# Performance work log

Measured on AMD Instinct MI355X. Metric: run time of the kernel, lower is better.

Reference implementation:

```python
import jax, jax.numpy as jnp
import numpy as np

N_USER = 100000
N_ITEM = 50000
N_EDGE = 400000
D_IN = 128
N_HEADS = 4
D_HEAD = 32


def setup_inputs() -> dict:
    key = jax.random.key(0)
    ks = jax.random.split(key, 10)
    s = 1.0 / np.sqrt(D_IN)
    return {
        "h_user": jax.random.normal(ks[0], (N_USER, D_IN), jnp.float32),
        "h_item": jax.random.normal(ks[1], (N_ITEM, D_IN), jnp.float32),
        "edge_user": jax.random.randint(ks[2], (N_EDGE,), 0, N_USER),
        "edge_item": jax.random.randint(ks[3], (N_EDGE,), 0, N_ITEM),
        "user_w_qs": jax.random.normal(ks[4], (N_HEADS, D_IN, D_HEAD), jnp.float32) * s,
        "user_w_ks": jax.random.normal(ks[5], (N_HEADS, D_IN, D_HEAD), jnp.float32) * s,
        "user_w_vs": jax.random.normal(ks[6], (N_HEADS, D_IN, D_HEAD), jnp.float32) * s,
        "item_w_qs": jax.random.normal(ks[7], (N_HEADS, D_IN, D_HEAD), jnp.float32) * s,
        "item_w_ks": jax.random.normal(ks[8], (N_HEADS, D_IN, D_HEAD), jnp.float32) * s,
        "item_w_vs": jax.random.normal(ks[9], (N_HEADS, D_IN, D_HEAD), jnp.float32) * s,
    }


def _segment_softmax(logit, seg, num_segments):
    m = jax.ops.segment_max(logit, seg, num_segments=num_segments)
    e = jnp.exp(logit - m[seg])
    s = jax.ops.segment_sum(e, seg, num_segments=num_segments)
    return e / s[seg]


def _attend(src_idx, dst_idx, h_src, h_dst, w_qs, w_ks, w_vs, n_dst):
    # per-head projections: [H, n, d_head]
    q = jnp.einsum("nd,hde->hne", h_dst, w_qs)
    k = jnp.einsum("nd,hde->hne", h_src, w_ks)
    v = jnp.einsum("nd,hde->hne", h_src, w_vs)
    # per-edge logits: [H, E]
    logit = jnp.sum(q[:, dst_idx] * k[:, src_idx], axis=-1)
    att = jax.vmap(lambda l: _segment_softmax(l, dst_idx, n_dst))(logit)
    # sparse adj @ v == segment-sum of attention-weighted source values
    msg = att[..., None] * v[:, src_idx]  # [H, E, d_head]
    z = jax.vmap(lambda m: jax.ops.segment_sum(m, dst_idx, num_segments=n_dst))(msg)
    z = jax.nn.relu(z)  # nonlinear per head, then merge (concat)
    return jnp.transpose(z, (1, 0, 2)).reshape(n_dst, -1)


def reference(h_user, h_item, edge_user, edge_item,
              user_w_qs, user_w_ks, user_w_vs,
              item_w_qs, item_w_ks, item_w_vs):
    # i2u: items -> users (dst = users)
    z_user = _attend(edge_item, edge_user, h_item, h_user,
                     user_w_qs, item_w_ks, item_w_vs, N_USER)
    # u2i: users -> items (dst = items)
    z_item = _attend(edge_user, edge_item, h_user, h_item,
                     item_w_qs, user_w_ks, user_w_vs, N_ITEM)
    return (z_user, z_item)
```

## Files before the change

### kernel.cpp

```cpp
#include <hip/hip_runtime.h>
#include <hip/hip_fp16.h>


typedef unsigned short u16;
typedef float f32x4 __attribute__((ext_vector_type(4)));
typedef short bf16x8 __attribute__((ext_vector_type(8)));

#define NU_C    100000
#define NI_C    50000
#define E_C     400000
#define D_IN    128
#define D_HEAD  32
#define N_HEADS 4

#define PROJ_ROWS 64

#define SCAN_T  256
#define SCAN_E  1024

__device__ __forceinline__ float bf2f(u16 b) {
    return __uint_as_float(((unsigned)b) << 16);
}

__device__ __forceinline__ u16 f2bf_rn(float x) {
    unsigned u = __float_as_uint(x);
    u += 0x7FFFu + ((u >> 16) & 1u);
    return (u16)(u >> 16);
}

__device__ __forceinline__ u16 f2h(float x) {
    return __half_as_ushort(__float2half(x));
}
__device__ __forceinline__ float h2f(u16 b) {
    return __half2float(__ushort_as_half(b));
}

__global__ void detect_dtypes(const void* __restrict__ h,
                              const void* __restrict__ eu,
                              int* __restrict__ flags) {
    if (threadIdx.x != 0 || blockIdx.x != 0) return;
    const u16* hw = (const u16*)h;
    int cnt = 0;
    for (int i = 0; i < 128; ++i) {
        unsigned ex = (hw[2 * i] >> 7) & 0xFFu;
        if (ex >= 118u && ex <= 137u) cnt++;
    }
    flags[0] = (cnt >= 64) ? 1 : 0;
    const int* ew = (const int*)eu;
    int nz = 0;
    for (int i = 0; i < 256; ++i)
        if (ew[2 * i + 1] != 0) nz++;
    flags[1] = (nz == 0) ? 1 : 0;
    flags[2] = 0;
    flags[3] = 0;
}

__global__ void decode_hist(const int* __restrict__ e_user,
                            const int* __restrict__ e_item,
                            int* __restrict__ du, int* __restrict__ di,
                            int* __restrict__ degU, int* __restrict__ degI,
                            int* __restrict__ flags) {
    int g = blockIdx.x * 256 + threadIdx.x;
    if (g >= E_C) return;
    int is64 = flags[1];
    int u = is64 ? e_user[2 * g] : e_user[g];
    int i = is64 ? e_item[2 * g] : e_item[g];
    if ((unsigned)u >= (unsigned)NU_C) { atomicOr(&flags[3], 1); u = 0; }
    if ((unsigned)i >= (unsigned)NI_C) { atomicOr(&flags[3], 1); i = 0; }
    du[g] = u;
    di[g] = i;
    atomicAdd(&degU[u], 1);
    atomicAdd(&degI[i], 1);
}

__global__ __launch_bounds__(256)
void wtrans(const void* __restrict__ w0, const void* __restrict__ w1,
            const void* __restrict__ w2, const void* __restrict__ w3,
            const void* __restrict__ w4, const void* __restrict__ w5,
            u16* __restrict__ wthi, u16* __restrict__ wtlo,
            const int* __restrict__ flags) {
    int b = blockIdx.x;
    int m = b >> 6;
    int f = (b & 63) * 256 + threadIdx.x;
    const void* ws[6] = { w0, w1, w2, w3, w4, w5 };
    const void* wp = ws[m];
    int head = f >> 12, d = (f >> 5) & 127, e = f & 31;
    float x;
    if (flags[0]) x = bf2f(((const u16*)wp)[f]);
    else          x = ((const float*)wp)[f];
    u16 h = f2bf_rn(x);
    u16 l = f2bf_rn(x - bf2f(h));
    int o = m * 16384 + (head * 32 + e) * 128 + d;
    wthi[o] = h;
    wtlo[o] = l;
}

__global__ __launch_bounds__(SCAN_T)
void scan_pass1(const int* __restrict__ degU, int* __restrict__ offsU,
                int* __restrict__ partU, int nU, int sbU,
                const int* __restrict__ degI, int* __restrict__ offsI,
                int* __restrict__ partI, int nI) {
    __shared__ int tsum[SCAN_T];
    int t = threadIdx.x, b = blockIdx.x;
    const int* deg; int* offs; int* partials; int n; int lb;
    if (b < sbU) { deg = degU; offs = offsU; partials = partU; n = nU; lb = b; }
    else         { deg = degI; offs = offsI; partials = partI; n = nI; lb = b - sbU; }
    int idx = lb * SCAN_E + t * 4;
    int v0 = 0, v1 = 0, v2 = 0, v3 = 0;
    if (idx + 3 < n) {
        v0 = deg[idx]; v1 = deg[idx + 1]; v2 = deg[idx + 2]; v3 = deg[idx + 3];
    } else {
        if (idx     < n) v0 = deg[idx];
        if (idx + 1 < n) v1 = deg[idx + 1];
        if (idx + 2 < n) v2 = deg[idx + 2];
        if (idx + 3 < n) v3 = deg[idx + 3];
    }
    int s = v0 + v1 + v2 + v3;
    tsum[t] = s;
    __syncthreads();
#pragma unroll
    for (int o = 1; o < SCAN_T; o <<= 1) {
        int x = (t >= o) ? tsum[t - o] : 0;
        __syncthreads();
        tsum[t] += x;
        __syncthreads();
    }
    int run = tsum[t] - s;
    if (idx     < n) offs[idx]     = run;             run += v0;
    if (idx + 1 < n) offs[idx + 1] = run;             run += v1;
    if (idx + 2 < n) offs[idx + 2] = run;             run += v2;
    if (idx + 3 < n) offs[idx + 3] = run;
    if (t == SCAN_T - 1) partials[lb] = tsum[t];
}

__global__ __launch_bounds__(SCAN_T)
void scan_pass2(int* __restrict__ partU, int sbU, int* __restrict__ offsU, int nU,
                int* __restrict__ partI, int sbI, int* __restrict__ offsI, int nI) {
    __shared__ int tsum[SCAN_T];
    int t = threadIdx.x;
    int* partials; int nb; int* offs; int n;
    if (blockIdx.x == 0) { partials = partU; nb = sbU; offs = offsU; n = nU; }
    else                 { partials = partI; nb = sbI; offs = offsI; n = nI; }
    int v = (t < nb) ? partials[t] : 0;
    tsum[t] = v;
    __syncthreads();
#pragma unroll
    for (int o = 1; o < SCAN_T; o <<= 1) {
        int x = (t >= o) ? tsum[t - o] : 0;
        __syncthreads();
        tsum[t] += x;
        __syncthreads();
    }
    if (t < nb) partials[t] = tsum[t] - v;
    if (t == SCAN_T - 1) offs[n] = tsum[t];
}

__global__ __launch_bounds__(SCAN_T)
void scan_pass3(int* __restrict__ offsU, const int* __restrict__ partU,
                int nU, int sbU,
                int* __restrict__ offsI, const int* __restrict__ partI, int nI) {
    int t = threadIdx.x, b = blockIdx.x;
    int* offs; const int* partials; int n; int lb;
    if (b < sbU) { offs = offsU; partials = partU; n = nU; lb = b; }
    else         { offs = offsI; partials = partI; n = nI; lb = b - sbU; }
    int add = partials[lb];
    int idx = lb * SCAN_E + t * 4;
#pragma unroll
    for (int i = 0; i < 4; ++i)
        if (idx + i < n) offs[idx + i] += add;
}

__global__ void scatter2(const int* __restrict__ du, const int* __restrict__ di,
                         const int* __restrict__ offsU, int* __restrict__ cntU,
                         int* __restrict__ csrU,
                         const int* __restrict__ offsI, int* __restrict__ cntI,
                         int* __restrict__ csrI, int egrid) {
    int b = blockIdx.x;
    int g = (b >= egrid ? b - egrid : b) * 256 + threadIdx.x;
    if (g >= E_C) return;
    if (b < egrid) {
        int d = du[g];
        int pos = offsU[d] + atomicAdd(&cntU[d], 1);
        csrU[pos] = di[g];
    } else {
        int d = di[g];
        int pos = offsI[d] + atomicAdd(&cntI[d], 1);
        csrI[pos] = du[g];
    }
}

__global__ __launch_bounds__(256)
void proj3(const void* __restrict__ h0, const u16* __restrict__ wth0,
           const u16* __restrict__ wtl0, u16* __restrict__ o0, int N0, int pg0,
           const void* __restrict__ h1, const u16* __restrict__ wth1,
           const u16* __restrict__ wtl1, u16* __restrict__ o1, int N1, int pg1,
           const void* __restrict__ h2, const u16* __restrict__ wth2,
           const u16* __restrict__ wtl2, u16* __restrict__ o2, int N2,
           const int* __restrict__ flags) {
    __shared__ u16 Hhi[PROJ_ROWS * 32], Hlo[PROJ_ROWS * 32];
    __shared__ u16 Bhi[128 * 32],       Blo[128 * 32];

    const int b = blockIdx.x;
    const void* hraw; const u16* wth; const u16* wtl; u16* out; int N; int lb;
    if (b < pg0)            { hraw = h0; wth = wth0; wtl = wtl0; out = o0; N = N0; lb = b; }
    else if (b < pg0 + pg1) { hraw = h1; wth = wth1; wtl = wtl1; out = o1; N = N1; lb = b - pg0; }
    else                    { hraw = h2; wth = wth2; wtl = wtl2; out = o2; N = N2; lb = b - pg0 - pg1; }

    const int t = threadIdx.x;
    const int n0 = lb * PROJ_ROWS;
    const int isbf = flags[0];

    const int srow = t >> 2, sq = t & 3;
    const int sgn = min(n0 + srow, N - 1);
    const int hbase = srow * 32 + ((sq ^ ((srow >> 1) & 3)) << 3);
    const int wj = t >> 1, wh = t & 1;
    const int wb0 = wj * 32 + (((wh * 2)     ^ ((wj >> 1) & 3)) << 3);
    const int wb1 = wj * 32 + (((wh * 2 + 1) ^ ((wj >> 1) & 3)) << 3);
    const int w = t >> 6, l = t & 63;
    const int lr = l & 15, lk = l >> 4;
    const int sc = (lk ^ ((lr >> 1) & 3)) << 3;

    f32x4 acc[4][2];
#pragma unroll
    for (int rt = 0; rt < 4; ++rt)
#pragma unroll
        for (int ci = 0; ci < 2; ++ci) {
            acc[rt][ci].x = 0.f; acc[rt][ci].y = 0.f;
            acc[rt][ci].z = 0.f; acc[rt][ci].w = 0.f;
        }

#define COMPUTE_STEP                                                           \
    do {                                                                       \
        bf16x8 fAh[4], fAl[4], fBh[2], fBl[2];                                 \
        _Pragma("unroll")                                                      \
        for (int rt = 0; rt < 4; ++rt) {                                       \
            int ar = (rt * 16 + lr) * 32 + sc;                                 \
            fAh[rt] = *(const bf16x8*)&Hhi[ar];                                \
            fAl[rt] = *(const bf16x8*)&Hlo[ar];                                \
        }                                                                      \
        _Pragma("unroll")                                                      \
        for (int ci = 0; ci < 2; ++ci) {                                       \
            int jr = ((w * 2 + ci) * 16 + lr) * 32 + sc;                       \
            fBh[ci] = *(const bf16x8*)&Bhi[jr];                                \
            fBl[ci] = *(const bf16x8*)&Blo[jr];                                \
        }                                                                      \
        _Pragma("unroll")                                                      \
        for (int rt = 0; rt < 4; ++rt)                                         \
        _Pragma("unroll")                                                      \
        for (int ci = 0; ci < 2; ++ci) {                                       \
            acc[rt][ci] = __builtin_amdgcn_mfma_f32_16x16x32_bf16(             \
                fAl[rt], fBh[ci], acc[rt][ci], 0, 0, 0);                       \
            acc[rt][ci] = __builtin_amdgcn_mfma_f32_16x16x32_bf16(             \
                fAh[rt], fBl[ci], acc[rt][ci], 0, 0, 0);                       \
            acc[rt][ci] = __builtin_amdgcn_mfma_f32_16x16x32_bf16(             \
                fAh[rt], fBh[ci], acc[rt][ci], 0, 0, 0);                       \
        }                                                                      \
    } while (0)

    if (!isbf) {
        const float* hp = (const float*)hraw;
        f32x4 rh0, rh1; bf16x8 rwh0, rwh1, rwl0, rwl1;
#define PLOAD(KC)                                                              \
        do {                                                                   \
            const float* hq = hp + (size_t)sgn * D_IN + (KC) * 32 + sq * 8;    \
            rh0 = *(const f32x4*)hq;                                           \
            rh1 = *(const f32x4*)(hq + 4);                                     \
            const u16* wp = wth + wj * 128 + (KC) * 32 + wh * 16;              \
            rwh0 = *(const bf16x8*)wp;  rwh1 = *(const bf16x8*)(wp + 8);       \
            const u16* lp = wtl + wj * 128 + (KC) * 32 + wh * 16;              \
            rwl0 = *(const bf16x8*)lp;  rwl1 = *(const bf16x8*)(lp + 8);       \
        } while (0)
        PLOAD(0);
        for (int kc = 0; kc < 4; ++kc) {
            if (kc) __syncthreads();
            bf16x8 hi8, lo8;
#pragma unroll
            for (int i = 0; i < 4; ++i) {
                u16 hh = f2bf_rn(rh0[i]);
                hi8[i] = (short)hh;
                lo8[i] = (short)f2bf_rn(rh0[i] - bf2f(hh));
            }
#pragma unroll
            for (int i = 0; i < 4; ++i) {
                u16 hh = f2bf_rn(rh1[i]);
                hi8[4 + i] = (short)hh;
                lo8[4 + i] = (short)f2bf_rn(rh1[i] - bf2f(hh));
            }
            *(bf16x8*)&Hhi[hbase] = hi8;
            *(bf16x8*)&Hlo[hbase] = lo8;
            *(bf16x8*)&Bhi[wb0] = rwh0;
            *(bf16x8*)&Bhi[wb1] = rwh1;
            *(bf16x8*)&Blo[wb0] = rwl0;
            *(bf16x8*)&Blo[wb1] = rwl1;
            __syncthreads();
            if (kc < 3) PLOAD(kc + 1);
            COMPUTE_STEP;
        }
#undef PLOAD
    } else {
        for (int kc = 0; kc < 4; ++kc) {
            if (kc) __syncthreads();
            bf16x8 hv = *(const bf16x8*)((const u16*)hraw
                        + (size_t)sgn * D_IN + kc * 32 + sq * 8);
            bf16x8 z;
#pragma unroll
            for (int i = 0; i < 8; ++i) z[i] = 0;
            *(bf16x8*)&Hhi[hbase] = hv;
            *(bf16x8*)&Hlo[hbase] = z;
            const u16* wp = wth + wj * 128 + kc * 32 + wh * 16;
            const u16* lp = wtl + wj * 128 + kc * 32 + wh * 16;
            *(bf16x8*)&Bhi[wb0] = *(const bf16x8*)wp;
            *(bf16x8*)&Bhi[wb1] = *(const bf16x8*)(wp + 8);
            *(bf16x8*)&Blo[wb0] = *(const bf16x8*)lp;
            *(bf16x8*)&Blo[wb1] = *(const bf16x8*)(lp + 8);
            __syncthreads();
            COMPUTE_STEP;
        }
    }
#undef COMPUTE_STEP

#pragma unroll
    for (int rt = 0; rt < 4; ++rt) {
#pragma unroll
        for (int r = 0; r < 4; ++r) {
            int n = n0 + rt * 16 + lk * 4 + r;
            if (n < N) {
#pragma unroll
                for (int ci = 0; ci < 2; ++ci)
                    out[(size_t)n * 128 + w * 32 + ci * 16 + lr] =
                        f2h(acc[rt][ci][r]);
            }
        }
    }
}

__global__ __launch_bounds__(256)
void gather64(const int* __restrict__ offs, const int* __restrict__ csr,
              const u16* __restrict__ q,
              const u16* __restrict__ k,
              const u16* __restrict__ v,
              float* __restrict__ out,
              int Ndst, const int* __restrict__ flags) {
    int g = blockIdx.x * 256 + threadIdx.x;
    int dst = g >> 6;
    if (dst >= Ndst) return;
    int l  = g & 63;
    int eh = l >> 5;
    int sl = l & 31;
    float* op = out + (size_t)dst * 128 + sl * 4;

    if (flags[3]) {
        if (eh == 0) {
            f32x4 d64; d64.x = d64.y = d64.z = d64.w = 64.0f;
            *(f32x4*)op = d64;
        }
        return;
    }

    ushort4 qu = *(const ushort4*)(q + (size_t)dst * 128 + sl * 4);
    f32x4 qv;
    qv.x = h2f(qu.x); qv.y = h2f(qu.y); qv.z = h2f(qu.z); qv.w = h2f(qu.w);
    f32x4 acc; acc.x = acc.y = acc.z = acc.w = 0.f;
    float ssum = 0.f;

    int e0 = offs[dst], e1 = offs[dst + 1];
    int e = e0 + eh;
    for (; e + 2 < e1; e += 4) {
        int s0 = csr[e];
        int s1 = csr[e + 2];
        ushort4 ku0 = *(const ushort4*)(k + (size_t)s0 * 128 + sl * 4);
        ushort4 ku1 = *(const ushort4*)(k + (size_t)s1 * 128 + sl * 4);
        ushort4 vu0 = *(const ushort4*)(v + (size_t)s0 * 128 + sl * 4);
        ushort4 vu1 = *(const ushort4*)(v + (size_t)s1 * 128 + sl * 4);
        float d0 = qv.x * h2f(ku0.x) + qv.y * h2f(ku0.y)
                 + qv.z * h2f(ku0.z) + qv.w * h2f(ku0.w);
        float d1 = qv.x * h2f(ku1.x) + qv.y * h2f(ku1.y)
                 + qv.z * h2f(ku1.z) + qv.w * h2f(ku1.w);
        d0 += __shfl_xor(d0, 1);  d1 += __shfl_xor(d1, 1);
        d0 += __shfl_xor(d0, 2);  d1 += __shfl_xor(d1, 2);
        d0 += __shfl_xor(d0, 4);  d1 += __shfl_xor(d1, 4);
        float ev0 = __expf(fminf(fmaxf(d0, -80.f), 80.f));
        float ev1 = __expf(fminf(fmaxf(d1, -80.f), 80.f));
        ssum += ev0 + ev1;
        acc.x += ev0 * h2f(vu0.x) + ev1 * h2f(vu1.x);
        acc.y += ev0 * h2f(vu0.y) + ev1 * h2f(vu1.y);
        acc.z += ev0 * h2f(vu0.z) + ev1 * h2f(vu1.z);
        acc.w += ev0 * h2f(vu0.w) + ev1 * h2f(vu1.w);
    }
    if (e < e1) {
        int s = csr[e];
        ushort4 ku = *(const ushort4*)(k + (size_t)s * 128 + sl * 4);
        ushort4 vu = *(const ushort4*)(v + (size_t)s * 128 + sl * 4);
        float d = qv.x * h2f(ku.x) + qv.y * h2f(ku.y)
                + qv.z * h2f(ku.z) + qv.w * h2f(ku.w);
        d += __shfl_xor(d, 1);
        d += __shfl_xor(d, 2);
        d += __shfl_xor(d, 4);
        float ev = __expf(fminf(fmaxf(d, -80.f), 80.f));
        ssum += ev;
        acc.x += ev * h2f(vu.x); acc.y += ev * h2f(vu.y);
        acc.z += ev * h2f(vu.z); acc.w += ev * h2f(vu.w);
    }
    ssum  += __shfl_xor(ssum, 32);
    acc.x += __shfl_xor(acc.x, 32);
    acc.y += __shfl_xor(acc.y, 32);
    acc.z += __shfl_xor(acc.z, 32);
    acc.w += __shfl_xor(acc.w, 32);
    if (eh == 0) {
        float inv = (ssum > 0.f) ? (1.f / ssum) : 0.f;
        f32x4 o;
        o.x = fmaxf(acc.x * inv, 0.f);
        o.y = fmaxf(acc.y * inv, 0.f);
        o.z = fmaxf(acc.z * inv, 0.f);
        o.w = fmaxf(acc.w * inv, 0.f);
        *(f32x4*)op = o;
    }
}

__global__ void fill_diag(float* __restrict__ out, int n) {
    int g = blockIdx.x * 256 + threadIdx.x;
    if (g < n) out[g] = 48.0f;
}

extern "C" void kernel_launch(void* const* d_in, const int* in_sizes, int n_in,
                              void* d_out, int out_size, void* d_ws, size_t ws_size,
                              hipStream_t stream) {
    const void* h_user    = d_in[0];
    const void* h_item    = d_in[1];
    const int*  edge_user = (const int*)d_in[2];
    const int*  edge_item = (const int*)d_in[3];
    const void* u_wq = d_in[4];
    const void* u_wk = d_in[5];
    const void* u_wv = d_in[6];
    const void* i_wq = d_in[7];
    const void* i_wk = d_in[8];
    const void* i_wv = d_in[9];

    const int NU = NU_C, NI = NI_C;

    size_t szBuf  = (((size_t)N_HEADS * NU * D_HEAD * 2) + 255) & ~(size_t)255;
    size_t szE    = (((size_t)E_C * 4) + 255) & ~(size_t)255;
    size_t szOffU = (((size_t)(NU + 1) * 4) + 255) & ~(size_t)255;
    size_t szOffI = (((size_t)(NI + 1) * 4) + 255) & ~(size_t)255;
    size_t szNU   = (((size_t)NU * 4) + 255) & ~(size_t)255;
    size_t szNI   = (((size_t)NI * 4) + 255) & ~(size_t)255;
    size_t szPart = 256 * 4;
    size_t szWt   = (size_t)6 * 16384 * 2;

    size_t off = 0;
    char* base = (char*)d_ws;
    u16* A       = (u16*)(base + off);   off += szBuf;
    u16* B       = (u16*)(base + off);   off += szBuf;
    u16* C       = (u16*)(base + off);   off += szBuf;
    int* du      = (int*)(base + off);   off += szE;
    int* di      = (int*)(base + off);   off += szE;
    int* csrU    = (int*)(base + off);   off += szE;
    int* csrI    = (int*)(base + off);   off += szE;
    int* offsU   = (int*)(base + off);   off += szOffU;
    int* offsI   = (int*)(base + off);   off += szOffI;
    int* partU   = (int*)(base + off);   off += szPart;
    int* partI   = (int*)(base + off);   off += szPart;
    u16* wthi    = (u16*)(base + off);   off += szWt;
    u16* wtlo    = (u16*)(base + off);   off += szWt;
    int* flags   = (int*)(base + off);   off += 256;
    size_t zoff = off;
    int* degU    = (int*)(base + off);   off += szNU;
    int* cntU    = (int*)(base + off);   off += szNU;
    int* degI    = (int*)(base + off);   off += szNI;
    int* cntI    = (int*)(base + off);   off += szNI;
    size_t need = off;

    if (need > ws_size) {
        fill_diag<<<(out_size + 255) / 256, 256, 0, stream>>>((float*)d_out, out_size);
        return;
    }

    int egrid = (E_C + 255) / 256;
    int pgU = (NU + PROJ_ROWS - 1) / PROJ_ROWS;
    int pgI = (NI + PROJ_ROWS - 1) / PROJ_ROWS;
    int sbU = (NU + SCAN_E - 1) / SCAN_E;
    int sbI = (NI + SCAN_E - 1) / SCAN_E;
    int ggU = (NU * 64 + 255) / 256;
    int ggI = (NI * 64 + 255) / 256;

    hipMemsetAsync(base + zoff, 0, need - zoff, stream);
    detect_dtypes<<<1, 64, 0, stream>>>(h_user, edge_user, flags);
    wtrans<<<6 * 64, 256, 0, stream>>>(u_wq, u_wk, u_wv, i_wq, i_wk, i_wv,
                                       wthi, wtlo, flags);
    decode_hist<<<egrid, 256, 0, stream>>>(edge_user, edge_item, du, di,
                                           degU, degI, flags);

    scan_pass1<<<sbU + sbI, SCAN_T, 0, stream>>>(degU, offsU, partU, NU, sbU,
                                                 degI, offsI, partI, NI);
    scan_pass2<<<2, SCAN_T, 0, stream>>>(partU, sbU, offsU, NU,
                                         partI, sbI, offsI, NI);
    scan_pass3<<<sbU + sbI, SCAN_T, 0, stream>>>(offsU, partU, NU, sbU,
                                                 offsI, partI, NI);

    scatter2<<<2 * egrid, 256, 0, stream>>>(du, di, offsU, cntU, csrU,
                                            offsI, cntI, csrI, egrid);

    proj3<<<pgU + 2 * pgI, 256, 0, stream>>>(
        h_user, wthi + 0 * 16384, wtlo + 0 * 16384, A, NU, pgU,
        h_item, wthi + 4 * 16384, wtlo + 4 * 16384, B, NI, pgI,
        h_item, wthi + 5 * 16384, wtlo + 5 * 16384, C, NI,
        flags);
    gather64<<<ggU, 256, 0, stream>>>(
        offsU, csrU, A, B, C, (float*)d_out, NU, flags);

    proj3<<<pgI + 2 * pgU, 256, 0, stream>>>(
        h_item, wthi + 3 * 16384, wtlo + 3 * 16384, A, NI, pgI,
        h_user, wthi + 1 * 16384, wtlo + 1 * 16384, B, NU, pgU,
        h_user, wthi + 2 * 16384, wtlo + 2 * 16384, C, NU,
        flags);
    gather64<<<ggI, 256, 0, stream>>>(
        offsI, csrI, A, B, C, (float*)d_out + (size_t)NU * 128, NI, flags);
}
```

Baseline: 399.3 us.

## Merge launches: fuse prep kernels, drop scan pass3, batch projections and gathers

Folds weight transposition and edge decode/histogram into one prep kernel and parallelizes dtype detection across a wavefront. Removes scan_pass3 by adding block partials on the fly in scatter and gather. Runs all six projections in one launch and both attention directions in one gather launch, so each launch has more blocks and the stream has fewer serial steps. In exchange it needs separate buffers for all six projection outputs, which raises workspace size and memory footprint.

Measured after the change: 366.8 us. 8.1% less time.

```diff
diff --git a/kernel.cpp b/kernel.cpp
--- a/kernel.cpp
+++ b/kernel.cpp
@@ -14,6 +14,9 @@
 #define N_HEADS 4
 
 #define PROJ_ROWS 64
+#define PGU 1563
+#define PGI 782
+#define WT_BLKS 384
 
 #define SCAN_T  256
 #define SCAN_E  1024
@@ -38,61 +41,72 @@
 __global__ void detect_dtypes(const void* __restrict__ h,
                               const void* __restrict__ eu,
                               int* __restrict__ flags) {
-    if (threadIdx.x != 0 || blockIdx.x != 0) return;
+    int t = threadIdx.x;
     const u16* hw = (const u16*)h;
     int cnt = 0;
-    for (int i = 0; i < 128; ++i) {
+#pragma unroll
+    for (int r = 0; r < 2; ++r) {
+        int i = t + r * 64;
         unsigned ex = (hw[2 * i] >> 7) & 0xFFu;
         if (ex >= 118u && ex <= 137u) cnt++;
     }
-    flags[0] = (cnt >= 64) ? 1 : 0;
     const int* ew = (const int*)eu;
     int nz = 0;
-    for (int i = 0; i < 256; ++i)
+#pragma unroll
+    for (int r = 0; r < 4; ++r) {
+        int i = t + r * 64;
         if (ew[2 * i + 1] != 0) nz++;
-    flags[1] = (nz == 0) ? 1 : 0;
-    flags[2] = 0;
-    flags[3] = 0;
-}
-
-__global__ void decode_hist(const int* __restrict__ e_user,
-                            const int* __restrict__ e_item,
-                            int* __restrict__ du, int* __restrict__ di,
-                            int* __restrict__ degU, int* __restrict__ degI,
-                            int* __restrict__ flags) {
-    int g = blockIdx.x * 256 + threadIdx.x;
-    if (g >= E_C) return;
-    int is64 = flags[1];
-    int u = is64 ? e_user[2 * g] : e_user[g];
-    int i = is64 ? e_item[2 * g] : e_item[g];
-    if ((unsigned)u >= (unsigned)NU_C) { atomicOr(&flags[3], 1); u = 0; }
-    if ((unsigned)i >= (unsigned)NI_C) { atomicOr(&flags[3], 1); i = 0; }
-    du[g] = u;
-    di[g] = i;
-    atomicAdd(&degU[u], 1);
-    atomicAdd(&degI[i], 1);
+    }
+#pragma unroll
+    for (int m = 1; m < 64; m <<= 1) {
+        cnt += __shfl_xor(cnt, m);
+        nz  += __shfl_xor(nz, m);
+    }
+    if (t == 0) {
+        flags[0] = (cnt >= 64) ? 1 : 0;
+        flags[1] = (nz == 0) ? 1 : 0;
+        flags[2] = 0;
+        flags[3] = 0;
+    }
 }
 
 __global__ __launch_bounds__(256)
-void wtrans(const void* __restrict__ w0, const void* __restrict__ w1,
-            const void* __restrict__ w2, const void* __restrict__ w3,
-            const void* __restrict__ w4, const void* __restrict__ w5,
-            u16* __restrict__ wthi, u16* __restrict__ wtlo,
-            const int* __restrict__ flags) {
+void prep(const void* __restrict__ w0, const void* __restrict__ w1,
+          const void* __restrict__ w2, const void* __restrict__ w3,
+          const void* __restrict__ w4, const void* __restrict__ w5,
+          u16* __restrict__ wthi, u16* __restrict__ wtlo,
+          const int* __restrict__ e_user, const int* __restrict__ e_item,
+          int* __restrict__ du, int* __restrict__ di,
+          int* __restrict__ degU, int* __restrict__ degI,
+          int* __restrict__ flags) {
     int b = blockIdx.x;
-    int m = b >> 6;
-    int f = (b & 63) * 256 + threadIdx.x;
-    const void* ws[6] = { w0, w1, w2, w3, w4, w5 };
-    const void* wp = ws[m];
-    int head = f >> 12, d = (f >> 5) & 127, e = f & 31;
-    float x;
-    if (flags[0]) x = bf2f(((const u16*)wp)[f]);
-    else          x = ((const float*)wp)[f];
-    u16 h = f2bf_rn(x);
-    u16 l = f2bf_rn(x - bf2f(h));
-    int o = m * 16384 + (head * 32 + e) * 128 + d;
-    wthi[o] = h;
-    wtlo[o] = l;
+    if (b < WT_BLKS) {
+        int m = b >> 6;
+        int f = (b & 63) * 256 + threadIdx.x;
+        const void* ws[6] = { w0, w1, w2, w3, w4, w5 };
+        const void* wp = ws[m];
+        int head = f >> 12, e = f & 31;
+        float x;
+        if (flags[0]) x = bf2f(((const u16*)wp)[f]);
+        else          x = ((const float*)wp)[f];
+        u16 h = f2bf_rn(x);
+        u16 l = f2bf_rn(x - bf2f(h));
+        int o = m * 16384 + (head * 32 + e) * 128 + ((f >> 5) & 127);
+        wthi[o] = h;
+        wtlo[o] = l;
+    } else {
+        int g = (b - WT_BLKS) * 256 + threadIdx.x;
+        if (g >= E_C) return;
+        int is64 = flags[1];
+        int u = is64 ? e_user[2 * g] : e_user[g];
+        int i = is64 ? e_item[2 * g] : e_item[g];
+        if ((unsigned)u >= (unsigned)NU_C) { atomicOr(&flags[3], 1); u = 0; }
+        if ((unsigned)i >= (unsigned)NI_C) { atomicOr(&flags[3], 1); i = 0; }
+        du[g] = u;
+        di[g] = i;
+        atomicAdd(&degU[u], 1);
+        atomicAdd(&degI[i], 1);
+    }
 }
 
 __global__ __launch_bounds__(SCAN_T)
@@ -134,13 +148,13 @@
 }
 
 __global__ __launch_bounds__(SCAN_T)
-void scan_pass2(int* __restrict__ partU, int sbU, int* __restrict__ offsU, int nU,
-                int* __restrict__ partI, int sbI, int* __restrict__ offsI, int nI) {
+void scan_pass2(int* __restrict__ partU, int sbU,
+                int* __restrict__ partI, int sbI) {
     __shared__ int tsum[SCAN_T];
     int t = threadIdx.x;
-    int* partials; int nb; int* offs; int n;
-    if (blockIdx.x == 0) { partials = partU; nb = sbU; offs = offsU; n = nU; }
-    else                 { partials = partI; nb = sbI; offs = offsI; n = nI; }
+    int* partials; int nb;
+    if (blockIdx.x == 0) { partials = partU; nb = sbU; }
+    else                 { partials = partI; nb = sbI; }
     int v = (t < nb) ? partials[t] : 0;
     tsum[t] = v;
     __syncthreads();
@@ -152,59 +166,57 @@
         __syncthreads();
     }
     if (t < nb) partials[t] = tsum[t] - v;
-    if (t == SCAN_T - 1) offs[n] = tsum[t];
-}
-
-__global__ __launch_bounds__(SCAN_T)
-void scan_pass3(int* __restrict__ offsU, const int* __restrict__ partU,
-                int nU, int sbU,
-                int* __restrict__ offsI, const int* __restrict__ partI, int nI) {
-    int t = threadIdx.x, b = blockIdx.x;
-    int* offs; const int* partials; int n; int lb;
-    if (b < sbU) { offs = offsU; partials = partU; n = nU; lb = b; }
-    else         { offs = offsI; partials = partI; n = nI; lb = b - sbU; }
-    int add = partials[lb];
-    int idx = lb * SCAN_E + t * 4;
-#pragma unroll
-    for (int i = 0; i < 4; ++i)
-        if (idx + i < n) offs[idx + i] += add;
 }
 
 __global__ void scatter2(const int* __restrict__ du, const int* __restrict__ di,
-                         const int* __restrict__ offsU, int* __restrict__ cntU,
-                         int* __restrict__ csrU,
-                         const int* __restrict__ offsI, int* __restrict__ cntI,
-                         int* __restrict__ csrI, int egrid) {
+                         const int* __restrict__ offsU, const int* __restrict__ partU,
+                         int* __restrict__ cntU, int* __restrict__ csrU,
+                         const int* __restrict__ offsI, const int* __restrict__ partI,
+                         int* __restrict__ cntI, int* __restrict__ csrI, int egrid) {
     int b = blockIdx.x;
     int g = (b >= egrid ? b - egrid : b) * 256 + threadIdx.x;
     if (g >= E_C) return;
     if (b < egrid) {
         int d = du[g];
-        int pos = offsU[d] + atomicAdd(&cntU[d], 1);
+        int pos = offsU[d] + partU[d >> 10] + atomicAdd(&cntU[d], 1);
         csrU[pos] = di[g];
     } else {
         int d = di[g];
-        int pos = offsI[d] + atomicAdd(&cntI[d], 1);
+        int pos = offsI[d] + partI[d >> 10] + atomicAdd(&cntI[d], 1);
         csrI[pos] = du[g];
     }
 }
 
 __global__ __launch_bounds__(256)
-void proj3(const void* __restrict__ h0, const u16* __restrict__ wth0,
-           const u16* __restrict__ wtl0, u16* __restrict__ o0, int N0, int pg0,
-           const void* __restrict__ h1, const u16* __restrict__ wth1,
-           const u16* __restrict__ wtl1, u16* __restrict__ o1, int N1, int pg1,
-           const void* __restrict__ h2, const u16* __restrict__ wth2,
-           const u16* __restrict__ wtl2, u16* __restrict__ o2, int N2,
+void proj6(const void* __restrict__ hu, const void* __restrict__ hi_,
+           const u16* __restrict__ wthi_, const u16* __restrict__ wtlo_,
+           u16* __restrict__ QU, u16* __restrict__ KI, u16* __restrict__ VI,
+           u16* __restrict__ QI, u16* __restrict__ KU, u16* __restrict__ VU,
            const int* __restrict__ flags) {
     __shared__ u16 Hhi[PROJ_ROWS * 32], Hlo[PROJ_ROWS * 32];
     __shared__ u16 Bhi[128 * 32],       Blo[128 * 32];
 
     const int b = blockIdx.x;
     const void* hraw; const u16* wth; const u16* wtl; u16* out; int N; int lb;
-    if (b < pg0)            { hraw = h0; wth = wth0; wtl = wtl0; out = o0; N = N0; lb = b; }
-    else if (b < pg0 + pg1) { hraw = h1; wth = wth1; wtl = wtl1; out = o1; N = N1; lb = b - pg0; }
-    else                    { hraw = h2; wth = wth2; wtl = wtl2; out = o2; N = N2; lb = b - pg0 - pg1; }
+    if (b < PGU) {
+        hraw = hu;  wth = wthi_ + 0 * 16384; wtl = wtlo_ + 0 * 16384;
+        out = QU; N = NU_C; lb = b;
+    } else if (b < PGU + PGI) {
+        hraw = hi_; wth = wthi_ + 4 * 16384; wtl = wtlo_ + 4 * 16384;
+        out = KI; N = NI_C; lb = b - PGU;
+    } else if (b < PGU + 2 * PGI) {
+        hraw = hi_; wth = wthi_ + 5 * 16384; wtl = wtlo_ + 5 * 16384;
+        out = VI; N = NI_C; lb = b - PGU - PGI;
+    } else if (b < PGU + 3 * PGI) {
+        hraw = hi_; wth = wthi_ + 3 * 16384; wtl = wtlo_ + 3 * 16384;
+        out = QI; N = NI_C; lb = b - PGU - 2 * PGI;
+    } else if (b < 2 * PGU + 3 * PGI) {
+        hraw = hu;  wth = wthi_ + 1 * 16384; wtl = wtlo_ + 1 * 16384;
+        out = KU; N = NU_C; lb = b - PGU - 3 * PGI;
+    } else {
+        hraw = hu;  wth = wthi_ + 2 * 16384; wtl = wtlo_ + 2 * 16384;
+        out = VU; N = NU_C; lb = b - 2 * PGU - 3 * PGI;
+    }
 
     const int t = threadIdx.x;
     const int n0 = lb * PROJ_ROWS;
@@ -335,13 +347,29 @@
 }
 
 __global__ __launch_bounds__(256)
-void gather64(const int* __restrict__ offs, const int* __restrict__ csr,
-              const u16* __restrict__ q,
-              const u16* __restrict__ k,
-              const u16* __restrict__ v,
-              float* __restrict__ out,
-              int Ndst, const int* __restrict__ flags) {
-    int g = blockIdx.x * 256 + threadIdx.x;
+void gather_both(const int* __restrict__ offsU, const int* __restrict__ partU,
+                 const int* __restrict__ csrU,
+                 const int* __restrict__ offsI, const int* __restrict__ partI,
+                 const int* __restrict__ csrI,
+                 const u16* __restrict__ QU, const u16* __restrict__ KI,
+                 const u16* __restrict__ VI,
+                 const u16* __restrict__ QI, const u16* __restrict__ KU,
+                 const u16* __restrict__ VU,
+                 float* __restrict__ outbase, const int* __restrict__ flags,
+                 int ggU) {
+    int b = blockIdx.x;
+    const int *offs, *part, *csr; const u16 *q, *k, *v;
+    float* out; int Ndst; int g;
+    if (b < ggU) {
+        offs = offsU; part = partU; csr = csrU;
+        q = QU; k = KI; v = VI; out = outbase; Ndst = NU_C;
+        g = b * 256 + threadIdx.x;
+    } else {
+        offs = offsI; part = partI; csr = csrI;
+        q = QI; k = KU; v = VU;
+        out = outbase + (size_t)NU_C * 128; Ndst = NI_C;
+        g = (b - ggU) * 256 + threadIdx.x;
+    }
     int dst = g >> 6;
     if (dst >= Ndst) return;
     int l  = g & 63;
@@ -363,7 +391,9 @@
     f32x4 acc; acc.x = acc.y = acc.z = acc.w = 0.f;
     float ssum = 0.f;
 
-    int e0 = offs[dst], e1 = offs[dst + 1];
+    int e0 = offs[dst] + part[dst >> 10];
+    int e1 = (dst + 1 == Ndst) ? E_C
+             : offs[dst + 1] + part[(dst + 1) >> 10];
     int e = e0 + eh;
     for (; e + 2 < e1; e += 4) {
         int s0 = csr[e];
@@ -438,7 +468,8 @@
 
     const int NU = NU_C, NI = NI_C;
 
-    size_t szBuf  = (((size_t)N_HEADS * NU * D_HEAD * 2) + 255) & ~(size_t)255;
+    size_t szBufU = (((size_t)NU * 128 * 2) + 255) & ~(size_t)255;
+    size_t szBufI = (((size_t)NI * 128 * 2) + 255) & ~(size_t)255;
     size_t szE    = (((size_t)E_C * 4) + 255) & ~(size_t)255;
     size_t szOffU = (((size_t)(NU + 1) * 4) + 255) & ~(size_t)255;
     size_t szOffI = (((size_t)(NI + 1) * 4) + 255) & ~(size_t)255;
@@ -449,9 +480,12 @@
 
     size_t off = 0;
     char* base = (char*)d_ws;
-    u16* A       = (u16*)(base + off);   off += szBuf;
-    u16* B       = (u16*)(base + off);   off += szBuf;
-    u16* C       = (u16*)(base + off);   off += szBuf;
+    u16* QU      = (u16*)(base + off);   off += szBufU;
+    u16* KI      = (u16*)(base + off);   off += szBufI;
+    u16* VI      = (u16*)(base + off);   off += szBufI;
+    u16* QI      = (u16*)(base + off);   off += szBufI;
+    u16* KU      = (u16*)(base + off);   off += szBufU;
+    u16* VU      = (u16*)(base + off);   off += szBufU;
     int* du      = (int*)(base + off);   off += szE;
     int* di      = (int*)(base + off);   off += szE;
     int* csrU    = (int*)(base + off);   off += szE;
@@ -476,8 +510,6 @@
     }
 
     int egrid = (E_C + 255) / 256;
-    int pgU = (NU + PROJ_ROWS - 1) / PROJ_ROWS;
-    int pgI = (NI + PROJ_ROWS - 1) / PROJ_ROWS;
     int sbU = (NU + SCAN_E - 1) / SCAN_E;
     int sbI = (NI + SCAN_E - 1) / SCAN_E;
     int ggU = (NU * 64 + 255) / 256;
@@ -485,34 +517,18 @@
 
     hipMemsetAsync(base + zoff, 0, need - zoff, stream);
     detect_dtypes<<<1, 64, 0, stream>>>(h_user, edge_user, flags);
-    wtrans<<<6 * 64, 256, 0, stream>>>(u_wq, u_wk, u_wv, i_wq, i_wk, i_wv,
-                                       wthi, wtlo, flags);
-    decode_hist<<<egrid, 256, 0, stream>>>(edge_user, edge_item, du, di,
-                                           degU, degI, flags);
-
+    prep<<<WT_BLKS + egrid, 256, 0, stream>>>(
+        u_wq, u_wk, u_wv, i_wq, i_wk, i_wv, wthi, wtlo,
+        edge_user, edge_item, du, di, degU, degI, flags);
     scan_pass1<<<sbU + sbI, SCAN_T, 0, stream>>>(degU, offsU, partU, NU, sbU,
                                                  degI, offsI, partI, NI);
-    scan_pass2<<<2, SCAN_T, 0, stream>>>(partU, sbU, offsU, NU,
-                                         partI, sbI, offsI, NI);
-    scan_pass3<<<sbU + sbI, SCAN_T, 0, stream>>>(offsU, partU, NU, sbU,
-                                                 offsI, partI, NI);
-
-    scatter2<<<2 * egrid, 256, 0, stream>>>(du, di, offsU, cntU, csrU,
-                                            offsI, cntI, csrI, egrid);
-
-    proj3<<<pgU + 2 * pgI, 256, 0, stream>>>(
-        h_user, wthi + 0 * 16384, wtlo + 0 * 16384, A, NU, pgU,
-        h_item, wthi + 4 * 16384, wtlo + 4 * 16384, B, NI, pgI,
-        h_item, wthi + 5 * 16384, wtlo + 5 * 16384, C, NI,
-        flags);
-    gather64<<<ggU, 256, 0, stream>>>(
-        offsU, csrU, A, B, C, (float*)d_out, NU, flags);
-
-    proj3<<<pgI + 2 * pgU, 256, 0, stream>>>(
-        h_item, wthi + 3 * 16384, wtlo + 3 * 16384, A, NI, pgI,
-        h_user, wthi + 1 * 16384, wtlo + 1 * 16384, B, NU, pgU,
-        h_user, wthi + 2 * 16384, wtlo + 2 * 16384, C, NU,
-        flags);
-    gather64<<<ggI, 256, 0, stream>>>(
-        offsI, csrI, A, B, C, (float*)d_out + (size_t)NU * 128, NI, flags);
-}
+    scan_pass2<<<2, SCAN_T, 0, stream>>>(partU, sbU, partI, sbI);
+    scatter2<<<2 * egrid, 256, 0, stream>>>(du, di,
+                                            offsU, partU, cntU, csrU,
+                                            offsI, partI, cntI, csrI, egrid);
+    proj6<<<3 * PGU + 3 * PGI, 256, 0, stream>>>(
+        h_user, h_item, wthi, wtlo, QU, KI, VI, QI, KU, VU, flags);
+    gather_both<<<ggU + ggI, 256, 0, stream>>>(
+        offsU, partU, csrU, offsI, partI, csrI,
+        QU, KI, VI, QI, KU, VU, (float*)d_out, flags, ggU);
+}
```
